# Kernel optimization log

Measured on AMD Instinct MI355X. Metric: run time of the kernel, lower is better.

The kernel has to match this reference:

```python
import jax, jax.numpy as jnp
import numpy as np

N = 100000
E = 3200000
F_IN = 512
NUM_CLASSES = 8
H1, C1 = 4, 8   # conv1: 4 heads, 8 channels each (concat -> 32)
H2, C2 = 1, NUM_CLASSES  # conv2: 1 head, mean (concat=False)
NEG_SLOPE = 0.2


def gat_conv(x, W, att_src, att_dst, bias, src, dst, num_nodes, concat):
    """PyG-style GATConv (eval mode, self-loops already in src/dst)."""
    H, C = att_src.shape
    xp = (x @ W).reshape(-1, H, C)              # [N, H, C]
    a_s = (xp * att_src[None]).sum(-1)           # [N, H]
    a_d = (xp * att_dst[None]).sum(-1)           # [N, H]
    e = jax.nn.leaky_relu(a_s[src] + a_d[dst], NEG_SLOPE)  # [E, H]
    # segment softmax over destination nodes (stable)
    e_max = jax.ops.segment_max(e, dst, num_segments=num_nodes)
    e = jnp.exp(e - e_max[dst])
    denom = jax.ops.segment_sum(e, dst, num_segments=num_nodes)
    alpha = e / denom[dst]                        # [E, H]
    msg = xp[src] * alpha[..., None]              # [E, H, C]
    out = jax.ops.segment_sum(msg, dst, num_segments=num_nodes)  # [N, H, C]
    if concat:
        out = out.reshape(num_nodes, H * C)
    else:
        out = out.mean(axis=1)
    return out + bias


def setup_inputs() -> dict:
    key = jax.random.key(0)
    ks = jax.random.split(key, 9)
    s = 0.1
    return {
        "x": jax.random.normal(ks[0], (N, F_IN), dtype=jnp.float32),
        "edge_index": jax.random.randint(ks[1], (2, E), 0, N, dtype=jnp.int32),
        "W1": jax.random.normal(ks[2], (F_IN, H1 * C1), dtype=jnp.float32) * s,
        "att_src1": jax.random.normal(ks[3], (H1, C1), dtype=jnp.float32) * s,
        "att_dst1": jax.random.normal(ks[4], (H1, C1), dtype=jnp.float32) * s,
        "b1": jnp.zeros((H1 * C1,), dtype=jnp.float32),
        "W2": jax.random.normal(ks[5], (H1 * C1, H2 * C2), dtype=jnp.float32) * s,
        "att_src2": jax.random.normal(ks[6], (H2, C2), dtype=jnp.float32) * s,
        "att_dst2": jax.random.normal(ks[7], (H2, C2), dtype=jnp.float32) * s,
        "b2": jnp.zeros((C2,), dtype=jnp.float32),
    }


def reference(x, edge_index, W1, att_src1, att_dst1, b1, W2, att_src2, att_dst2, b2):
    # PyG GATConv default add_self_loops=True
    loop = jnp.arange(N, dtype=edge_index.dtype)
    src = jnp.concatenate([edge_index[0], loop])
    dst = jnp.concatenate([edge_index[1], loop])
    # dropout is identity in eval mode
    h = jax.nn.elu(gat_conv(x, W1, att_src1, att_dst1, b1, src, dst, N, True))
    out = gat_conv(h, W2, att_src2, att_dst2, b2, src, dst, N, False)
    return out
```

## Files before the change

### kernel.cpp

```cpp
#include <hip/hip_runtime.h>

typedef unsigned short u16;
typedef unsigned int   u32;

#define NN  100000
#define EE  3200000
#define ETOT 3300000
#define FIN 512
#define NBUK 512
#define NPB  196
#define CAP  8192
#define TILE_A 8192
#define NBLK_A ((ETOT + TILE_A - 1) / TILE_A)
#define NBLK_G ((NN + 63) / 64)

typedef __attribute__((ext_vector_type(8))) short bfx8;
typedef __attribute__((ext_vector_type(4))) float f32x4;

__device__ __forceinline__ float bf2f(u16 u){ return __uint_as_float(((u32)u) << 16); }
__device__ __forceinline__ float lo16f(u32 v){ return __uint_as_float(v << 16); }
__device__ __forceinline__ float hi16f(u32 v){ return __uint_as_float(v & 0xffff0000u); }
__device__ __forceinline__ u16 f2bf(float f){
  u32 u = __float_as_uint(f);
  u += 0x7fffu + ((u >> 16) & 1u);
  return (u16)(u >> 16);
}
__device__ __forceinline__ u32 pack2(float a, float b){
  return ((u32)f2bf(b) << 16) | (u32)f2bf(a);
}
__device__ __forceinline__ u32 cvtpk(float a, float b){
  u32 r;
  asm("v_cvt_pk_bf16_f32 %0, %1, %2" : "=v"(r) : "v"(a), "v"(b));
  return r;
}

__device__ __forceinline__ void binA_body(int blk, const int* __restrict__ ei,
                                          u32* __restrict__ gcnt,
                                          u32* __restrict__ buk,
                                          u32* hcnt, u32* hbase){
  int t = threadIdx.x;
  hcnt[t] = 0; hcnt[t + 256] = 0;
  __syncthreads();
  int e0 = blk * TILE_A;
  u32 pk[32], meta[32];
  #pragma unroll
  for (int i = 0; i < 32; i++){
    int e = e0 + i*256 + t;
    if (e < ETOT){
      int s, d;
      if (e < EE){ s = ei[e]; d = ei[EE + e]; } else { s = e - EE; d = s; }
      u32 b = (u32)d / NPB;
      pk[i] = ((u32)(d - (int)b*NPB) << 17) | (u32)s;
      u32 r = atomicAdd(&hcnt[b], 1u);
      meta[i] = (b << 13) | r;
    } else meta[i] = 0xFFFFFFFFu;
  }
  __syncthreads();
  for (int q = t; q < NBUK; q += 256){
    u32 c = hcnt[q];
    if (c) hbase[q] = atomicAdd(&gcnt[q], c);
  }
  __syncthreads();
  #pragma unroll
  for (int i = 0; i < 32; i++){
    if (meta[i] != 0xFFFFFFFFu){
      u32 b = meta[i] >> 13, r = meta[i] & 8191u;
      buk[((u32)b << 13) + hbase[b] + r] = pk[i];
    }
  }
}

__device__ __forceinline__ void gemm_body(int gb,
    const float* __restrict__ x, const u16* __restrict__ WTb,
    const float* __restrict__ attS, const float* __restrict__ attD,
    u16* __restrict__ xp1, float* __restrict__ as1, float* __restrict__ ad1,
    u16* ws){
  int tid = threadIdx.x;
  int nb  = gb * 64;

  {
    int r = tid >> 3, seg = tid & 7;
    const uint4* src = (const uint4*)(WTb + r*FIN + seg*64);
    uint4* dst = (uint4*)(ws + r*520 + seg*64);
    #pragma unroll
    for (int i = 0; i < 8; i++) dst[i] = src[i];
  }
  __syncthreads();

  int lane = tid & 63, wid = tid >> 6;
  int m = lane & 15, quad = lane >> 4;
  int rowbase = wid * 16;
  int row = nb + rowbase + m; if (row >= NN) row = NN - 1;
  const float* xrow = x + (size_t)row * FIN + quad * 8;
  const u16* b0_base = ws + m * 520 + quad * 8;
  const u16* b1_base = b0_base + 16 * 520;

  f32x4 acc0 = {0.f, 0.f, 0.f, 0.f};
  f32x4 acc1 = {0.f, 0.f, 0.f, 0.f};

  union Ubf { bfx8 v; u32 u[4]; };

  #pragma unroll
  for (int kc = 0; kc < 4; kc++){
    float4 fx[8];
    #pragma unroll
    for (int ks = 0; ks < 4; ks++){
      const float4* g = (const float4*)(xrow + kc*128 + ks*32);
      fx[2*ks]   = g[0];
      fx[2*ks+1] = g[1];
    }
    #pragma unroll
    for (int ks = 0; ks < 4; ks++){
      Ubf ua;
      ua.u[0] = cvtpk(fx[2*ks].x,   fx[2*ks].y);
      ua.u[1] = cvtpk(fx[2*ks].z,   fx[2*ks].w);
      ua.u[2] = cvtpk(fx[2*ks+1].x, fx[2*ks+1].y);
      ua.u[3] = cvtpk(fx[2*ks+1].z, fx[2*ks+1].w);
      bfx8 b0 = *(const bfx8*)(b0_base + kc*128 + ks*32);
      bfx8 b1 = *(const bfx8*)(b1_base + kc*128 + ks*32);
      acc0 = __builtin_amdgcn_mfma_f32_16x16x32_bf16(ua.v, b0, acc0, 0, 0, 0);
      acc1 = __builtin_amdgcn_mfma_f32_16x16x32_bf16(ua.v, b1, acc1, 0, 0, 0);
    }
  }

  #pragma unroll
  for (int t = 0; t < 2; t++){
    f32x4 acc = t ? acc1 : acc0;
    int colg = t*16 + m;
    float aS = attS[colg], aD = attD[colg];
    #pragma unroll
    for (int r = 0; r < 4; r++){
      int node = nb + rowbase + quad*4 + r;
      float v = acc[r];
      if (node < NN) xp1[(size_t)node*32 + colg] = f2bf(v);
      float ps = v * aS, pd = v * aD;
      ps += __shfl_xor(ps, 1); ps += __shfl_xor(ps, 2); ps += __shfl_xor(ps, 4);
      pd += __shfl_xor(pd, 1); pd += __shfl_xor(pd, 2); pd += __shfl_xor(pd, 4);
      if ((m & 7) == 0 && node < NN){
        as1[node*4 + (colg >> 3)] = ps;
        ad1[node*4 + (colg >> 3)] = pd;
      }
    }
  }
}


__global__ void __launch_bounds__(256) k_fat(const int* __restrict__ ei,
    u32* __restrict__ gcnt, u32* __restrict__ buk,
    const float* __restrict__ x, const u16* __restrict__ WTb,
    const float* __restrict__ attS, const float* __restrict__ attD,
    u16* __restrict__ xp1, float* __restrict__ as1, float* __restrict__ ad1){
  __shared__ __align__(16) char sm[32 * 520 * 2];
  if (blockIdx.x < NBLK_A)
    binA_body(blockIdx.x, ei, gcnt, buk, (u32*)sm, (u32*)sm + NBUK);
  else
    gemm_body(blockIdx.x - NBLK_A, x, WTb, attS, attD, xp1, as1, ad1, (u16*)sm);
}

__global__ void __launch_bounds__(256) k_binA(const int* __restrict__ ei,
                                              u32* __restrict__ gcnt,
                                              u32* __restrict__ buk){
  __shared__ u32 sm2[NBUK*2];
  binA_body(blockIdx.x, ei, gcnt, buk, sm2, sm2 + NBUK);
}

__global__ void __launch_bounds__(256) k_gemm1(
    const float* __restrict__ x, const u16* __restrict__ WTb,
    const float* __restrict__ attS, const float* __restrict__ attD,
    u16* __restrict__ xp1, float* __restrict__ as1, float* __restrict__ ad1){
  __shared__ u16 ws[32 * 520];
  gemm_body(blockIdx.x, x, WTb, attS, attD, xp1, as1, ad1, ws);
}

__global__ void __launch_bounds__(256) k_scatterB(const u32* __restrict__ gcnt,
                                                  const u32* __restrict__ buk,
                                                  int2* __restrict__ range,
                                                  int* __restrict__ srcs){
  __shared__ u32 dcnt[NPB + 1];
  __shared__ u32 cur[NPB];
  __shared__ u32 red[256];
  int b = blockIdx.x, t = threadIdx.x;
  u32 acc = 0;
  for (int i = t; i < b; i += 256) acc += gcnt[i];
  red[t] = acc;
  if (t < NPB + 1) dcnt[t] = 0;
  __syncthreads();
  for (int o = 128; o > 0; o >>= 1){
    if (t < o) red[t] += red[t + o];
    __syncthreads();
  }
  u32 gb = red[0];
  u32 lo = (u32)b << 13;
  u32 hi = lo + gcnt[b];
  for (u32 j = lo + t; j < hi; j += 256)
    atomicAdd(&dcnt[(buk[j] >> 17) + 1], 1u);
  __syncthreads();
  for (int o = 1; o < 256; o <<= 1){
    u32 x = 0;
    if (t < NPB + 1 && t >= o) x = dcnt[t - o];
    __syncthreads();
    if (t < NPB + 1 && t >= o) dcnt[t] += x;
    __syncthreads();
  }
  if (t < NPB){
    u32 beg = gb + dcnt[t];
    cur[t] = beg;
    int node = b * NPB + t;
    if (node < NN){
      range[node] = make_int2((int)beg, (int)(gb + dcnt[t + 1]));
    }
  }
  __syncthreads();
  for (u32 j = lo + t; j < hi; j += 256){
    u32 p = buk[j];
    u32 pos = atomicAdd(&cur[p >> 17], 1u);
    srcs[pos] = (int)(p & 0x1FFFFu);
  }
}

__global__ void k_prep_w(const float* __restrict__ W1, u16* __restrict__ WTb,
                         u32* __restrict__ gcnt){
  int i = blockIdx.x*blockDim.x + threadIdx.x;
  if (i < NBUK) gcnt[i] = 0;
  if (i >= FIN*32) return;
  int k = i >> 5, c = i & 31;
  WTb[c*FIN + k] = f2bf(W1[i]);
}

__global__ void __launch_bounds__(256) k_agg1(
    const int2* __restrict__ range, const int* __restrict__ srcs,
    const u32* __restrict__ xp1u, const float* __restrict__ as1,
    const float* __restrict__ ad1, const float* __restrict__ b1,
    u32* __restrict__ hfeatu){
  int wid = (blockIdx.x * 256 + threadIdx.x) >> 6;
  if (wid >= NN) return;
  int lane = threadIdx.x & 63;
  int e = lane >> 4;
  int l = lane & 15;
  int h = l >> 2;
  int2 rr = range[wid];
  int beg = rr.x, end = rr.y;
  float ad = ad1[wid*4 + h];
  float num0 = 0.f, num1 = 0.f, den = 0.f;
  int j = beg + e;
  for (; j + 12 < end; j += 16){
    int s0 = srcs[j], s1 = srcs[j + 4], s2 = srcs[j + 8], s3 = srcs[j + 12];
    u32 v0 = xp1u[(size_t)s0*16 + l];
    u32 v1 = xp1u[(size_t)s1*16 + l];
    u32 v2 = xp1u[(size_t)s2*16 + l];
    u32 v3 = xp1u[(size_t)s3*16 + l];
    float z0 = as1[s0*4 + h] + ad;
    float z1 = as1[s1*4 + h] + ad;
    float z2 = as1[s2*4 + h] + ad;
    float z3 = as1[s3*4 + h] + ad;
    z0 = (z0 >= 0.f) ? z0 : 0.2f * z0;
    z1 = (z1 >= 0.f) ? z1 : 0.2f * z1;
    z2 = (z2 >= 0.f) ? z2 : 0.2f * z2;
    z3 = (z3 >= 0.f) ? z3 : 0.2f * z3;
    float w0 = __expf(z0), w1 = __expf(z1), w2 = __expf(z2), w3 = __expf(z3);
    num0 = fmaf(w0, lo16f(v0), num0); num1 = fmaf(w0, hi16f(v0), num1); den += w0;
    num0 = fmaf(w1, lo16f(v1), num0); num1 = fmaf(w1, hi16f(v1), num1); den += w1;
    num0 = fmaf(w2, lo16f(v2), num0); num1 = fmaf(w2, hi16f(v2), num1); den += w2;
    num0 = fmaf(w3, lo16f(v3), num0); num1 = fmaf(w3, hi16f(v3), num1); den += w3;
  }
  if (j + 4 < end){
    int s0 = srcs[j], s1 = srcs[j + 4];
    u32 v0 = xp1u[(size_t)s0*16 + l];
    u32 v1 = xp1u[(size_t)s1*16 + l];
    float z0 = as1[s0*4 + h] + ad;
    float z1 = as1[s1*4 + h] + ad;
    z0 = (z0 >= 0.f) ? z0 : 0.2f * z0;
    z1 = (z1 >= 0.f) ? z1 : 0.2f * z1;
    float w0 = __expf(z0), w1 = __expf(z1);
    num0 = fmaf(w0, lo16f(v0), num0); num1 = fmaf(w0, hi16f(v0), num1); den += w0;
    num0 = fmaf(w1, lo16f(v1), num0); num1 = fmaf(w1, hi16f(v1), num1); den += w1;
    j += 8;
  }
  for (; j < end; j += 4){
    int s0 = srcs[j];
    u32 v0 = xp1u[(size_t)s0*16 + l];
    float z0 = as1[s0*4 + h] + ad;
    z0 = (z0 >= 0.f) ? z0 : 0.2f * z0;
    float w0 = __expf(z0);
    num0 = fmaf(w0, lo16f(v0), num0); num1 = fmaf(w0, hi16f(v0), num1); den += w0;
  }
  num0 += __shfl_xor(num0, 16); num0 += __shfl_xor(num0, 32);
  num1 += __shfl_xor(num1, 16); num1 += __shfl_xor(num1, 32);
  den  += __shfl_xor(den, 16);  den  += __shfl_xor(den, 32);
  if (e == 0){
    float o0 = num0 / den + b1[2*l];
    float o1 = num1 / den + b1[2*l + 1];
    o0 = (o0 > 0.f) ? o0 : (__expf(o0) - 1.f);
    o1 = (o1 > 0.f) ? o1 : (__expf(o1) - 1.f);
    hfeatu[(size_t)wid*16 + l] = pack2(o0, o1);
  }
}

__global__ void k_feat2(const u16* __restrict__ hfeat, const float* __restrict__ W2,
                        const float* __restrict__ attS, const float* __restrict__ attD,
                        float* __restrict__ xp2, float* __restrict__ as2,
                        float* __restrict__ ad2){
  int n = blockIdx.x*blockDim.x + threadIdx.x;
  if (n >= NN) return;
  const u16* hr = hfeat + (size_t)n*32;
  float h[32];
  #pragma unroll
  for (int k = 0; k < 32; k++) h[k] = bf2f(hr[k]);
  float o[8];
  #pragma unroll
  for (int j = 0; j < 8; j++) o[j] = 0.f;
  #pragma unroll
  for (int k = 0; k < 32; k++){
    #pragma unroll
    for (int j = 0; j < 8; j++) o[j] = fmaf(h[k], W2[k*8 + j], o[j]);
  }
  float s = 0.f, d = 0.f;
  #pragma unroll
  for (int j = 0; j < 8; j++){
    xp2[(size_t)n*8 + j] = o[j];
    s = fmaf(o[j], attS[j], s);
    d = fmaf(o[j], attD[j], d);
  }
  as2[n] = s; ad2[n] = d;
}

__global__ void __launch_bounds__(256) k_agg2(
    const int2* __restrict__ range, const int* __restrict__ srcs,
    const float* __restrict__ xp2, const float* __restrict__ as2,
    const float* __restrict__ ad2, const float* __restrict__ b2,
    float* __restrict__ out){
  int wid = (blockIdx.x * 256 + threadIdx.x) >> 6;
  if (wid >= NN) return;
  int lane = threadIdx.x & 63;
  int p = lane >> 3, c = lane & 7;
  int2 rr = range[wid];
  int beg = rr.x, end = rr.y;
  float ad = ad2[wid];
  float num = 0.f, den = 0.f;
  int j = beg + p;
  for (; j + 24 < end; j += 32){
    int s0 = srcs[j], s1 = srcs[j + 8], s2 = srcs[j + 16], s3 = srcs[j + 24];
    float v0 = xp2[(size_t)s0*8 + c];
    float v1 = xp2[(size_t)s1*8 + c];
    float v2 = xp2[(size_t)s2*8 + c];
    float v3 = xp2[(size_t)s3*8 + c];
    float z0 = as2[s0] + ad;
    float z1 = as2[s1] + ad;
    float z2 = as2[s2] + ad;
    float z3 = as2[s3] + ad;
    z0 = (z0 >= 0.f) ? z0 : 0.2f * z0;
    z1 = (z1 >= 0.f) ? z1 : 0.2f * z1;
    z2 = (z2 >= 0.f) ? z2 : 0.2f * z2;
    z3 = (z3 >= 0.f) ? z3 : 0.2f * z3;
    float w0 = __expf(z0), w1 = __expf(z1), w2 = __expf(z2), w3 = __expf(z3);
    num = fmaf(w0, v0, num); den += w0;
    num = fmaf(w1, v1, num); den += w1;
    num = fmaf(w2, v2, num); den += w2;
    num = fmaf(w3, v3, num); den += w3;
  }
  if (j + 8 < end){
    int s0 = srcs[j], s1 = srcs[j + 8];
    float v0 = xp2[(size_t)s0*8 + c];
    float v1 = xp2[(size_t)s1*8 + c];
    float z0 = as2[s0] + ad;
    float z1 = as2[s1] + ad;
    z0 = (z0 >= 0.f) ? z0 : 0.2f * z0;
    z1 = (z1 >= 0.f) ? z1 : 0.2f * z1;
    float w0 = __expf(z0), w1 = __expf(z1);
    num = fmaf(w0, v0, num); den += w0;
    num = fmaf(w1, v1, num); den += w1;
    j += 16;
  }
  for (; j < end; j += 8){
    int s0 = srcs[j];
    float v0 = xp2[(size_t)s0*8 + c];
    float z0 = as2[s0] + ad;
    z0 = (z0 >= 0.f) ? z0 : 0.2f * z0;
    float w0 = __expf(z0);
    num = fmaf(w0, v0, num); den += w0;
  }
  num += __shfl_xor(num, 8);  den += __shfl_xor(den, 8);
  num += __shfl_xor(num, 16); den += __shfl_xor(den, 16);
  num += __shfl_xor(num, 32); den += __shfl_xor(den, 32);
  if (p == 0){
    out[(size_t)wid*8 + c] = num / den + b2[c];
  }
}

extern "C" void kernel_launch(void* const* d_in, const int* in_sizes, int n_in,
                              void* d_out, int out_size, void* d_ws, size_t ws_size,
                              hipStream_t stream){
  (void)in_sizes; (void)n_in; (void)out_size;
  const float* x   = (const float*)d_in[0];
  const int*   ei  = (const int*)d_in[1];
  const float* W1  = (const float*)d_in[2];
  const float* aS1 = (const float*)d_in[3];
  const float* aD1 = (const float*)d_in[4];
  const float* b1  = (const float*)d_in[5];
  const float* W2  = (const float*)d_in[6];
  const float* aS2 = (const float*)d_in[7];
  const float* aD2 = (const float*)d_in[8];
  const float* b2  = (const float*)d_in[9];
  float* out = (float*)d_out;

  char* w = (char*)d_ws;
  auto alloc = [&](size_t bytes) -> char* {
    char* p = w; w += (bytes + 15) & ~(size_t)15; return p;
  };

  int2*  range  = (int2*)alloc((size_t)NN*8);
  int*   srcs   = (int*)alloc((size_t)ETOT*4);
  u16*   xp1    = (u16*)alloc((size_t)NN*64);
  float* as1    = (float*)alloc((size_t)NN*16);
  float* ad1    = (float*)alloc((size_t)NN*16);
  u16*   hfeat  = (u16*)alloc((size_t)NN*64);
  float* xp2    = (float*)alloc((size_t)NN*32);
  float* as2    = (float*)alloc((size_t)NN*4);
  float* ad2    = (float*)alloc((size_t)NN*4);
  u16*   WTb    = (u16*)alloc(32*512*2);
  u32*   gcnt   = (u32*)alloc(NBUK*4);
  size_t base_need = (size_t)(w - (char*)d_ws);
  size_t buk_bytes = (size_t)NBUK * CAP * 4;
  bool overlap = (ws_size >= base_need + buk_bytes);

  u32* buk;
  if (overlap){
    buk = (u32*)alloc(buk_bytes);
  } else {
    buk = (u32*)xp1;
  }

  k_prep_w  <<<64, 256, 0, stream>>>(W1, WTb, gcnt);
  if (overlap){
    k_fat   <<<NBLK_A + NBLK_G, 256, 0, stream>>>(ei, gcnt, buk, x, WTb, aS1, aD1,
                                                  xp1, as1, ad1);
    k_scatterB<<<NBUK, 256, 0, stream>>>(gcnt, buk, range, srcs);
  } else {
    k_binA  <<<NBLK_A, 256, 0, stream>>>(ei, gcnt, buk);
    k_scatterB<<<NBUK, 256, 0, stream>>>(gcnt, buk, range, srcs);
    k_gemm1 <<<NBLK_G, 256, 0, stream>>>(x, WTb, aS1, aD1, xp1, as1, ad1);
  }
  k_agg1    <<<NN/4, 256, 0, stream>>>(range, srcs, (const u32*)xp1, as1, ad1, b1, (u32*)hfeat);
  k_feat2   <<<(NN+255)/256, 256, 0, stream>>>(hfeat, W2, aS2, aD2, xp2, as2, ad2);
  k_agg2    <<<NN/4, 256, 0, stream>>>(range, srcs, xp2, as2, ad2, b2, out);
}
```

Before: 468.0 us.

## Fuse scatter phase into fat kernel with atomic completion counter wait

Appends the scatterB blocks to the combined binning+GEMM launch. The scatter blocks spin on a global counter until all binning blocks have finished, so scatter work can overlap the tail of the GEMM blocks and one kernel launch is removed. The spin-wait depends on the binning blocks being scheduled before the scatter blocks and adds atomic polling. It also removes the kernel-boundary gap between the two phases.

```diff
diff --git a/kernel.cpp b/kernel.cpp
--- a/kernel.cpp
+++ b/kernel.cpp
@@ -144,17 +144,79 @@
   }
 }
 
+__device__ __forceinline__ void scatterB_body(int b, const u32* __restrict__ gcnt,
+                                              const u32* __restrict__ buk,
+                                              int2* __restrict__ range,
+                                              int* __restrict__ srcs,
+                                              u32* dcnt, u32* cur, u32* red){
+  int t = threadIdx.x;
+  u32 acc = 0;
+  for (int i = t; i < b; i += 256) acc += gcnt[i];
+  red[t] = acc;
+  if (t < NPB + 1) dcnt[t] = 0;
+  __syncthreads();
+  for (int o = 128; o > 0; o >>= 1){
+    if (t < o) red[t] += red[t + o];
+    __syncthreads();
+  }
+  u32 gb = red[0];
+  u32 lo = (u32)b << 13;
+  u32 hi = lo + gcnt[b];
+  for (u32 j = lo + t; j < hi; j += 256)
+    atomicAdd(&dcnt[(buk[j] >> 17) + 1], 1u);
+  __syncthreads();
+  for (int o = 1; o < 256; o <<= 1){
+    u32 x = 0;
+    if (t < NPB + 1 && t >= o) x = dcnt[t - o];
+    __syncthreads();
+    if (t < NPB + 1 && t >= o) dcnt[t] += x;
+    __syncthreads();
+  }
+  if (t < NPB){
+    u32 beg = gb + dcnt[t];
+    cur[t] = beg;
+    int node = b * NPB + t;
+    if (node < NN){
+      range[node] = make_int2((int)beg, (int)(gb + dcnt[t + 1]));
+    }
+  }
+  __syncthreads();
+  for (u32 j = lo + t; j < hi; j += 256){
+    u32 p = buk[j];
+    u32 pos = atomicAdd(&cur[p >> 17], 1u);
+    srcs[pos] = (int)(p & 0x1FFFFu);
+  }
+}
+
 
 __global__ void __launch_bounds__(256) k_fat(const int* __restrict__ ei,
-    u32* __restrict__ gcnt, u32* __restrict__ buk,
+    u32* __restrict__ gcnt, u32* __restrict__ buk, u32* __restrict__ done,
     const float* __restrict__ x, const u16* __restrict__ WTb,
     const float* __restrict__ attS, const float* __restrict__ attD,
-    u16* __restrict__ xp1, float* __restrict__ as1, float* __restrict__ ad1){
+    u16* __restrict__ xp1, float* __restrict__ as1, float* __restrict__ ad1,
+    int2* __restrict__ range, int* __restrict__ srcs){
   __shared__ __align__(16) char sm[32 * 520 * 2];
-  if (blockIdx.x < NBLK_A)
-    binA_body(blockIdx.x, ei, gcnt, buk, (u32*)sm, (u32*)sm + NBUK);
-  else
-    gemm_body(blockIdx.x - NBLK_A, x, WTb, attS, attD, xp1, as1, ad1, (u16*)sm);
+  int bid = blockIdx.x;
+  if (bid < NBLK_A){
+    binA_body(bid, ei, gcnt, buk, (u32*)sm, (u32*)sm + NBUK);
+    __syncthreads();
+    if (threadIdx.x == 0){
+      __threadfence();
+      atomicAdd(done, 1u);
+    }
+  } else if (bid < NBLK_A + NBLK_G){
+    gemm_body(bid - NBLK_A, x, WTb, attS, attD, xp1, as1, ad1, (u16*)sm);
+  } else {
+    if (threadIdx.x == 0){
+      while (atomicAdd(done, 0u) < (u32)NBLK_A) __builtin_amdgcn_s_sleep(2);
+      __threadfence();
+    }
+    __syncthreads();
+    u32* dcnt = (u32*)sm;
+    u32* cur  = dcnt + (NPB + 1);
+    u32* red  = cur + NPB;
+    scatterB_body(bid - NBLK_A - NBLK_G, gcnt, buk, range, srcs, dcnt, cur, red);
+  }
 }
 
 __global__ void __launch_bounds__(256) k_binA(const int* __restrict__ ei,
@@ -179,49 +241,14 @@
   __shared__ u32 dcnt[NPB + 1];
   __shared__ u32 cur[NPB];
   __shared__ u32 red[256];
-  int b = blockIdx.x, t = threadIdx.x;
-  u32 acc = 0;
-  for (int i = t; i < b; i += 256) acc += gcnt[i];
-  red[t] = acc;
-  if (t < NPB + 1) dcnt[t] = 0;
-  __syncthreads();
-  for (int o = 128; o > 0; o >>= 1){
-    if (t < o) red[t] += red[t + o];
-    __syncthreads();
-  }
-  u32 gb = red[0];
-  u32 lo = (u32)b << 13;
-  u32 hi = lo + gcnt[b];
-  for (u32 j = lo + t; j < hi; j += 256)
-    atomicAdd(&dcnt[(buk[j] >> 17) + 1], 1u);
-  __syncthreads();
-  for (int o = 1; o < 256; o <<= 1){
-    u32 x = 0;
-    if (t < NPB + 1 && t >= o) x = dcnt[t - o];
-    __syncthreads();
-    if (t < NPB + 1 && t >= o) dcnt[t] += x;
-    __syncthreads();
-  }
-  if (t < NPB){
-    u32 beg = gb + dcnt[t];
-    cur[t] = beg;
-    int node = b * NPB + t;
-    if (node < NN){
-      range[node] = make_int2((int)beg, (int)(gb + dcnt[t + 1]));
-    }
-  }
-  __syncthreads();
-  for (u32 j = lo + t; j < hi; j += 256){
-    u32 p = buk[j];
-    u32 pos = atomicAdd(&cur[p >> 17], 1u);
-    srcs[pos] = (int)(p & 0x1FFFFu);
-  }
+  scatterB_body(blockIdx.x, gcnt, buk, range, srcs, dcnt, cur, red);
 }
 
 __global__ void k_prep_w(const float* __restrict__ W1, u16* __restrict__ WTb,
-                         u32* __restrict__ gcnt){
+                         u32* __restrict__ gcnt, u32* __restrict__ done){
   int i = blockIdx.x*blockDim.x + threadIdx.x;
   if (i < NBUK) gcnt[i] = 0;
+  if (i == NBUK) *done = 0;
   if (i >= FIN*32) return;
   int k = i >> 5, c = i & 31;
   WTb[c*FIN + k] = f2bf(W1[i]);
@@ -419,6 +446,7 @@
   float* ad2    = (float*)alloc((size_t)NN*4);
   u16*   WTb    = (u16*)alloc(32*512*2);
   u32*   gcnt   = (u32*)alloc(NBUK*4);
+  u32*   done   = (u32*)alloc(16);
   size_t base_need = (size_t)(w - (char*)d_ws);
   size_t buk_bytes = (size_t)NBUK * CAP * 4;
   bool overlap = (ws_size >= base_need + buk_bytes);
@@ -430,11 +458,12 @@
     buk = (u32*)xp1;
   }
 
-  k_prep_w  <<<64, 256, 0, stream>>>(W1, WTb, gcnt);
+  k_prep_w  <<<64, 256, 0, stream>>>(W1, WTb, gcnt, done);
   if (overlap){
-    k_fat   <<<NBLK_A + NBLK_G, 256, 0, stream>>>(ei, gcnt, buk, x, WTb, aS1, aD1,
-                                                  xp1, as1, ad1);
-    k_scatterB<<<NBUK, 256, 0, stream>>>(gcnt, buk, range, srcs);
+    k_fat   <<<NBLK_A + NBLK_G + NBUK, 256, 0, stream>>>(ei, gcnt, buk, done,
+                                                         x, WTb, aS1, aD1,
+                                                         xp1, as1, ad1,
+                                                         range, srcs);
   } else {
     k_binA  <<<NBLK_A, 256, 0, stream>>>(ei, gcnt, buk);
     k_scatterB<<<NBUK, 256, 0, stream>>>(gcnt, buk, range, srcs);
```

Result: slower. 548.1 us (+17.1%).
